# Kernel optimization log

Hardware: AMD Instinct MI355X
Metric: run time of the kernel (lower is better)

## Reference

```python
import jax, jax.numpy as jnp
import numpy as np

EPS = jnp.finfo(jnp.float32).eps


def setup_inputs() -> dict:
    key = jax.random.key(0)
    k0, k1, k2 = jax.random.split(key, 3)
    B, N = 1, 4194304
    cloud_t0 = jax.random.normal(k0, (B, N, 3), dtype=jnp.float32)
    cloud_t1 = jax.random.normal(k1, (B, N, 3), dtype=jnp.float32)
    weights = jax.random.uniform(k2, (B, N), dtype=jnp.float32)
    return {"cloud_t0": cloud_t0, "cloud_t1": cloud_t1, "weights": weights}


def reference(cloud_t0, cloud_t1, weights):
    # use_epsilon_on_weights = False branch
    count_nonzero = jnp.sum(weights > 0.0, axis=-1)
    not_enough_points = count_nonzero < 3
    weights = weights + (not_enough_points.astype(weights.dtype) * EPS)[:, None]

    cum_wts = jnp.sum(weights, axis=-1)                      # (B,)
    w = weights[:, :, None]                                   # (B,N,1)
    mx = jnp.sum(cloud_t0 * w, axis=1) / cum_wts[:, None]     # (B,3) weighted centroid
    my = jnp.sum(cloud_t1 * w, axis=1) / cum_wts[:, None]
    Xc = cloud_t0 - mx[:, None, :]
    Yc = cloud_t1 - my[:, None, :]
    # weighted cross-covariance: (B,3,3)
    Sxy = jnp.einsum('bno,bni->boi', Yc * w, Xc) / cum_wts[:, None, None]

    U, D, Vh = jnp.linalg.svd(Sxy, full_matrices=False)       # torch.svd returns V = Vh^T
    V = jnp.swapaxes(Vh, -1, -2)

    # rank via torch.linalg.matrix_rank default tol: max_sv * max(m,n) * eps
    tol = D.max(axis=-1) * 3 * EPS
    rank = jnp.sum(D > tol[:, None], axis=-1)

    det_S = jnp.linalg.det(Sxy)
    det_mul = jnp.linalg.det(U) * jnp.linalg.det(V)
    sign_full = jnp.where(det_S < 0.0, -1.0, 1.0)             # rank == 3 case
    sign_def = jnp.where(jnp.isclose(det_mul, -1.0), -1.0, 1.0)  # rank == 2 case
    s = jnp.where(rank > 2, sign_full, sign_def)              # (B,)

    # R = U @ diag(1,1,s) @ V^T
    diag = jnp.stack([jnp.ones_like(s), jnp.ones_like(s), s], axis=-1)  # (B,3)
    R = jnp.einsum('boc,bc,bic->boi', U, diag, V)             # (B,3,3)
    t = my - jnp.einsum('boc,bc->bo', R, mx)                  # (B,3)

    B = R.shape[0]
    R4 = jnp.concatenate([R, jnp.zeros((B, 1, 3), R.dtype)], axis=1)    # (B,4,3)
    t4 = jnp.concatenate([t, jnp.ones((B, 1), t.dtype)], axis=-1)       # (B,4)
    T = jnp.concatenate([R4, t4[:, :, None]], axis=-1)        # (B,4,4)
    return T, not_enough_points
```

## Files before the change

### kernel.cpp

```cpp
#include <hip/hip_runtime.h>
#include <math.h>

#define NACC 32

typedef float f4 __attribute__((ext_vector_type(4)));

__device__ __forceinline__ void accum_point(float w, float x0, float x1, float x2,
                                            float y0, float y1, float y2, float* a) {
    a[0] += (w > 0.0f) ? 1.0f : 0.0f;
    a[1] += w;
    a[2] = fmaf(w, x0, a[2]); a[3] = fmaf(w, x1, a[3]); a[4] = fmaf(w, x2, a[4]);
    float wy0 = w * y0, wy1 = w * y1, wy2 = w * y2;
    a[5] += wy0; a[6] += wy1; a[7] += wy2;
    a[8]  = fmaf(wy0, x0, a[8]);  a[9]  = fmaf(wy0, x1, a[9]);  a[10] = fmaf(wy0, x2, a[10]);
    a[11] = fmaf(wy1, x0, a[11]); a[12] = fmaf(wy1, x1, a[12]); a[13] = fmaf(wy1, x2, a[13]);
    a[14] = fmaf(wy2, x0, a[14]); a[15] = fmaf(wy2, x1, a[15]); a[16] = fmaf(wy2, x2, a[16]);
    a[17] += x0; a[18] += x1; a[19] += x2;
    a[20] += y0; a[21] += y1; a[22] += y2;
    a[23] = fmaf(y0, x0, a[23]); a[24] = fmaf(y0, x1, a[24]); a[25] = fmaf(y0, x2, a[25]);
    a[26] = fmaf(y1, x0, a[26]); a[27] = fmaf(y1, x1, a[27]); a[28] = fmaf(y1, x2, a[28]);
    a[29] = fmaf(y2, x0, a[29]); a[30] = fmaf(y2, x1, a[30]); a[31] = fmaf(y2, x2, a[31]);
}

__global__ __launch_bounds__(256) void kabsch_reduce(
    const float* __restrict__ c0, const float* __restrict__ c1,
    const float* __restrict__ w, int N, float* __restrict__ partials, int nblocks) {
    __shared__ float wred[4][NACC];

    float a[NACC];
    #pragma unroll
    for (int i = 0; i < NACC; ++i) a[i] = 0.0f;

    const int t = threadIdx.x;
    const int lane = t & 63, wave = t >> 6;
    const f4* __restrict__ A4 = (const f4*)c0;
    const f4* __restrict__ B4 = (const f4*)c1;
    const f4* __restrict__ W4 = (const f4*)w;

    const int ngrp = N >> 2;
    const int stride = gridDim.x << 8;
    for (int g = (blockIdx.x << 8) + t; g < ngrp; g += stride) {
        const f4* pa = A4 + 3 * (size_t)g;
        const f4* pb = B4 + 3 * (size_t)g;
        const f4* pw = W4 + (size_t)g;
        f4 a0, a1, a2, b0, b1, b2, vw;
        asm volatile("global_load_dwordx4 %0, %1, off"           : "=v"(a0) : "v"(pa));
        asm volatile("global_load_dwordx4 %0, %1, off offset:16" : "=v"(a1) : "v"(pa));
        asm volatile("global_load_dwordx4 %0, %1, off offset:32" : "=v"(a2) : "v"(pa));
        asm volatile("global_load_dwordx4 %0, %1, off"           : "=v"(b0) : "v"(pb));
        asm volatile("global_load_dwordx4 %0, %1, off offset:16" : "=v"(b1) : "v"(pb));
        asm volatile("global_load_dwordx4 %0, %1, off offset:32" : "=v"(b2) : "v"(pb));
        asm volatile("global_load_dwordx4 %0, %1, off"           : "=v"(vw) : "v"(pw));
        asm volatile("s_waitcnt vmcnt(0)" ::: "memory");
        __builtin_amdgcn_sched_barrier(0);
        accum_point(vw.x, a0.x, a0.y, a0.z, b0.x, b0.y, b0.z, a);
        accum_point(vw.y, a0.w, a1.x, a1.y, b0.w, b1.x, b1.y, a);
        accum_point(vw.z, a1.z, a1.w, a2.x, b1.z, b1.w, b2.x, a);
        accum_point(vw.w, a2.y, a2.z, a2.w, b2.y, b2.z, b2.w, a);
    }
    if (blockIdx.x == 0 && t == 0) {
        for (int i = (N >> 2) << 2; i < N; ++i)
            accum_point(w[i], c0[3*i], c0[3*i+1], c0[3*i+2],
                        c1[3*i], c1[3*i+1], c1[3*i+2], a);
    }

    {
        int hi;
        hi = lane & 1;
        #pragma unroll
        for (int i = 0; i < 16; ++i) {
            float send = hi ? a[i] : a[i + 16];
            float recv = __shfl_xor(send, 1, 64);
            a[i] = (hi ? a[i + 16] : a[i]) + recv;
        }
        hi = lane & 2;
        #pragma unroll
        for (int i = 0; i < 8; ++i) {
            float send = hi ? a[i] : a[i + 8];
            float recv = __shfl_xor(send, 2, 64);
            a[i] = (hi ? a[i + 8] : a[i]) + recv;
        }
        hi = lane & 4;
        #pragma unroll
        for (int i = 0; i < 4; ++i) {
            float send = hi ? a[i] : a[i + 4];
            float recv = __shfl_xor(send, 4, 64);
            a[i] = (hi ? a[i + 4] : a[i]) + recv;
        }
        hi = lane & 8;
        #pragma unroll
        for (int i = 0; i < 2; ++i) {
            float send = hi ? a[i] : a[i + 2];
            float recv = __shfl_xor(send, 8, 64);
            a[i] = (hi ? a[i + 2] : a[i]) + recv;
        }
        hi = lane & 16;
        {
            float send = hi ? a[0] : a[1];
            float recv = __shfl_xor(send, 16, 64);
            a[0] = (hi ? a[1] : a[0]) + recv;
        }
        a[0] += __shfl_xor(a[0], 32, 64);
    }
    if (lane < 32) {
        int acc = ((lane & 1) << 4) | ((lane & 2) << 2) | (lane & 4)
                | ((lane & 8) >> 2) | ((lane & 16) >> 4);
        wred[wave][acc] = a[0];
    }
    __syncthreads();
    if (t < NACC)
        partials[t * nblocks + blockIdx.x] =
            wred[0][t] + wred[1][t] + wred[2][t] + wred[3][t];
}

__device__ __forceinline__ double det3(const double m[3][3]) {
    return m[0][0] * (m[1][1] * m[2][2] - m[1][2] * m[2][1])
         - m[0][1] * (m[1][0] * m[2][2] - m[1][2] * m[2][0])
         + m[0][2] * (m[1][0] * m[2][1] - m[1][1] * m[2][0]);
}

__global__ __launch_bounds__(256) void kabsch_finalize(
    const float* __restrict__ partials, int nblocks, int N, float* __restrict__ out) {
    double d[NACC];
    #pragma unroll
    for (int i = 0; i < NACC; ++i) d[i] = 0.0;
    for (int m = threadIdx.x; m < nblocks; m += 256) {
        #pragma unroll
        for (int i = 0; i < NACC; ++i)
            d[i] += (double)partials[i * nblocks + m];
    }
    #pragma unroll
    for (int off = 32; off > 0; off >>= 1) {
        #pragma unroll
        for (int i = 0; i < NACC; ++i) d[i] += __shfl_down(d[i], off, 64);
    }
    __shared__ double sm[4][NACC];
    int wave = threadIdx.x >> 6, lane = threadIdx.x & 63;
    if (lane == 0) {
        #pragma unroll
        for (int i = 0; i < NACC; ++i) sm[wave][i] = d[i];
    }
    __syncthreads();
    if (threadIdx.x != 0) return;
    #pragma unroll
    for (int i = 0; i < NACC; ++i) d[i] = sm[0][i] + sm[1][i] + sm[2][i] + sm[3][i];

    const double EPSF = (double)1.1920929e-7f;
    double cnt = d[0];
    double W = d[1];
    double swx[3] = { d[2], d[3], d[4] };
    double swy[3] = { d[5], d[6], d[7] };
    double swyx[9];
    for (int i = 0; i < 9; ++i) swyx[i] = d[8 + i];
    bool nep = cnt < 3.0;
    if (nep) {
        W += EPSF * (double)N;
        for (int i = 0; i < 3; ++i) { swx[i] += EPSF * d[17 + i]; swy[i] += EPSF * d[20 + i]; }
        for (int i = 0; i < 9; ++i) swyx[i] += EPSF * d[23 + i];
    }

    double mx[3], my[3];
    for (int i = 0; i < 3; ++i) { mx[i] = swx[i] / W; my[i] = swy[i] / W; }
    double S[3][3];
    for (int o = 0; o < 3; ++o)
        for (int i = 0; i < 3; ++i)
            S[o][i] = swyx[o * 3 + i] / W - my[o] * mx[i];

    double Bm[3][3], V[3][3];
    for (int i = 0; i < 3; ++i)
        for (int j = 0; j < 3; ++j) {
            double acc = 0.0;
            for (int k = 0; k < 3; ++k) acc += S[k][i] * S[k][j];
            Bm[i][j] = acc;
            V[i][j] = (i == j) ? 1.0 : 0.0;
        }
    for (int sweep = 0; sweep < 30; ++sweep) {
        double off2 = Bm[0][1]*Bm[0][1] + Bm[0][2]*Bm[0][2] + Bm[1][2]*Bm[1][2];
        double diag2 = Bm[0][0]*Bm[0][0] + Bm[1][1]*Bm[1][1] + Bm[2][2]*Bm[2][2];
        if (off2 <= diag2 * 1e-32 + 1e-300) break;
        for (int pair = 0; pair < 3; ++pair) {
            int p = (pair == 2) ? 1 : 0;
            int q = (pair == 0) ? 1 : 2;
            double apq = Bm[p][q];
            if (fabs(apq) < 1e-300) continue;
            double theta = (Bm[q][q] - Bm[p][p]) / (2.0 * apq);
            double tt = ((theta >= 0.0) ? 1.0 : -1.0) / (fabs(theta) + sqrt(1.0 + theta * theta));
            double c = 1.0 / sqrt(1.0 + tt * tt);
            double sn = tt * c;
            for (int k = 0; k < 3; ++k) {
                double bkp = Bm[k][p], bkq = Bm[k][q];
                Bm[k][p] = c * bkp - sn * bkq;
                Bm[k][q] = sn * bkp + c * bkq;
            }
            for (int k = 0; k < 3; ++k) {
                double bpk = Bm[p][k], bqk = Bm[q][k];
                Bm[p][k] = c * bpk - sn * bqk;
                Bm[q][k] = sn * bpk + c * bqk;
            }
            for (int k = 0; k < 3; ++k) {
                double vkp = V[k][p], vkq = V[k][q];
                V[k][p] = c * vkp - sn * vkq;
                V[k][q] = sn * vkp + c * vkq;
            }
        }
    }
    double lam[3] = { Bm[0][0], Bm[1][1], Bm[2][2] };
    for (int i = 0; i < 2; ++i)
        for (int j = i + 1; j < 3; ++j)
            if (lam[j] > lam[i]) {
                double tl = lam[i]; lam[i] = lam[j]; lam[j] = tl;
                for (int k = 0; k < 3; ++k) { double tv = V[k][i]; V[k][i] = V[k][j]; V[k][j] = tv; }
            }
    double sig[3];
    for (int i = 0; i < 3; ++i) sig[i] = sqrt(fmax(lam[i], 0.0));

    double U[3][3];
    for (int i = 0; i < 3; ++i) {
        double u0 = S[0][0]*V[0][i] + S[0][1]*V[1][i] + S[0][2]*V[2][i];
        double u1 = S[1][0]*V[0][i] + S[1][1]*V[1][i] + S[1][2]*V[2][i];
        double u2 = S[2][0]*V[0][i] + S[2][1]*V[1][i] + S[2][2]*V[2][i];
        double nrm = sqrt(u0*u0 + u1*u1 + u2*u2);
        if (nrm > 1e-150) {
            U[0][i] = u0 / nrm; U[1][i] = u1 / nrm; U[2][i] = u2 / nrm;
        } else if (i == 0) {
            U[0][0] = 1.0; U[1][0] = 0.0; U[2][0] = 0.0;
        } else if (i == 1) {
            double e0 = (fabs(U[0][0]) < 0.9) ? 1.0 : 0.0;
            double e1 = 1.0 - e0;
            double dp = e0 * U[0][0] + e1 * U[1][0];
            double v0 = e0 - dp * U[0][0], v1 = e1 - dp * U[1][0], v2 = -dp * U[2][0];
            double n2 = sqrt(v0*v0 + v1*v1 + v2*v2);
            U[0][1] = v0 / n2; U[1][1] = v1 / n2; U[2][1] = v2 / n2;
        } else {
            U[0][2] = U[1][0]*U[2][1] - U[2][0]*U[1][1];
            U[1][2] = U[2][0]*U[0][1] - U[0][0]*U[2][1];
            U[2][2] = U[0][0]*U[1][1] - U[1][0]*U[0][1];
        }
    }

    double tol = sig[0] * 3.0 * EPSF;
    int rank = (sig[0] > tol) + (sig[1] > tol) + (sig[2] > tol);
    double detS = det3(S);
    double det_mul = det3(U) * det3(V);
    double sign_full = (detS < 0.0) ? -1.0 : 1.0;
    double sign_def = (fabs(det_mul + 1.0) <= 1.00001e-5) ? -1.0 : 1.0;
    double s = (rank > 2) ? sign_full : sign_def;

    double R[3][3];
    for (int o = 0; o < 3; ++o)
        for (int i = 0; i < 3; ++i)
            R[o][i] = U[o][0]*V[i][0] + U[o][1]*V[i][1] + s * U[o][2]*V[i][2];
    double tv[3];
    for (int o = 0; o < 3; ++o)
        tv[o] = my[o] - (R[o][0]*mx[0] + R[o][1]*mx[1] + R[o][2]*mx[2]);

    for (int o = 0; o < 3; ++o) {
        out[o * 4 + 0] = (float)R[o][0];
        out[o * 4 + 1] = (float)R[o][1];
        out[o * 4 + 2] = (float)R[o][2];
        out[o * 4 + 3] = (float)tv[o];
    }
    out[12] = 0.0f; out[13] = 0.0f; out[14] = 0.0f; out[15] = 1.0f;
    out[16] = nep ? 1.0f : 0.0f;
}

extern "C" void kernel_launch(void* const* d_in, const int* in_sizes, int n_in,
                              void* d_out, int out_size, void* d_ws, size_t ws_size,
                              hipStream_t stream) {
    const float* c0 = (const float*)d_in[0];
    const float* c1 = (const float*)d_in[1];
    const float* w  = (const float*)d_in[2];
    float* out = (float*)d_out;
    int N = in_sizes[2];

    int ngrp = N >> 2;
    int blocks = (ngrp + 255) >> 8;
    if (blocks > 4096) blocks = 4096;
    if (blocks < 1) blocks = 1;
    size_t need = (size_t)blocks * NACC * sizeof(float);
    if (need > ws_size) {
        blocks = (int)(ws_size / (NACC * sizeof(float)));
        if (blocks < 1) blocks = 1;
    }
    float* partials = (float*)d_ws;

    kabsch_reduce<<<blocks, 256, 0, stream>>>(c0, c1, w, N, partials, blocks);
    kabsch_finalize<<<1, 256, 0, stream>>>(partials, blocks, N, out);
}
```

Measured before the change: 155.3 us.

## Fuse reduce and finalize kernels with last-block ticket and parallel partial sum

```diff
diff --git a/kernel.cpp b/kernel.cpp
--- a/kernel.cpp
+++ b/kernel.cpp
@@ -22,9 +22,16 @@
     a[29] = fmaf(y2, x0, a[29]); a[30] = fmaf(y2, x1, a[30]); a[31] = fmaf(y2, x2, a[31]);
 }
 
-__global__ __launch_bounds__(256) void kabsch_reduce(
+__device__ __forceinline__ double det3(const double m[3][3]) {
+    return m[0][0] * (m[1][1] * m[2][2] - m[1][2] * m[2][1])
+         - m[0][1] * (m[1][0] * m[2][2] - m[1][2] * m[2][0])
+         + m[0][2] * (m[1][0] * m[2][1] - m[1][1] * m[2][0]);
+}
+
+__global__ __launch_bounds__(256) void kabsch_fused(
     const float* __restrict__ c0, const float* __restrict__ c1,
-    const float* __restrict__ w, int N, float* __restrict__ partials, int nblocks) {
+    const float* __restrict__ w, int N, float* __restrict__ partials, int nblocks,
+    unsigned* __restrict__ ticket, float* __restrict__ out) {
     __shared__ float wred[4][NACC];
 
     float a[NACC];
@@ -111,39 +118,53 @@
     if (t < NACC)
         partials[t * nblocks + blockIdx.x] =
             wred[0][t] + wred[1][t] + wred[2][t] + wred[3][t];
-}
-
-__device__ __forceinline__ double det3(const double m[3][3]) {
-    return m[0][0] * (m[1][1] * m[2][2] - m[1][2] * m[2][1])
-         - m[0][1] * (m[1][0] * m[2][2] - m[1][2] * m[2][0])
-         + m[0][2] * (m[1][0] * m[2][1] - m[1][1] * m[2][0]);
-}
-
-__global__ __launch_bounds__(256) void kabsch_finalize(
-    const float* __restrict__ partials, int nblocks, int N, float* __restrict__ out) {
+
+    __threadfence();
+    __syncthreads();
+    __shared__ unsigned amlast;
+    if (t == 0) amlast = atomicAdd(ticket, 1u);
+    __syncthreads();
+    if (amlast != (unsigned)(nblocks - 1)) return;
+    __threadfence();
+
+    double dd[8];
+    #pragma unroll
+    for (int i = 0; i < 8; ++i) dd[i] = 0.0;
+    if ((nblocks & 3) == 0) {
+        const int nb4 = nblocks >> 2;
+        const f4* __restrict__ p4 = (const f4*)partials;
+        #pragma unroll
+        for (int i = 0; i < 8; ++i) {
+            int row = (wave << 3) + i;
+            for (int j = lane; j < nb4; j += 64) {
+                f4 v = p4[row * nb4 + j];
+                dd[i] += ((double)v.x + (double)v.y) + ((double)v.z + (double)v.w);
+            }
+        }
+    } else {
+        #pragma unroll
+        for (int i = 0; i < 8; ++i) {
+            int row = (wave << 3) + i;
+            for (int j = lane; j < nblocks; j += 64)
+                dd[i] += (double)partials[row * nblocks + j];
+        }
+    }
+    #pragma unroll
+    for (int off = 32; off > 0; off >>= 1) {
+        #pragma unroll
+        for (int i = 0; i < 8; ++i) dd[i] += __shfl_down(dd[i], off, 64);
+    }
+    __shared__ double sm[NACC];
+    if (lane == 0) {
+        #pragma unroll
+        for (int i = 0; i < 8; ++i) sm[(wave << 3) + i] = dd[i];
+    }
+    __syncthreads();
+    if (t != 0) return;
+
     double d[NACC];
     #pragma unroll
-    for (int i = 0; i < NACC; ++i) d[i] = 0.0;
-    for (int m = threadIdx.x; m < nblocks; m += 256) {
-        #pragma unroll
-        for (int i = 0; i < NACC; ++i)
-            d[i] += (double)partials[i * nblocks + m];
-    }
-    #pragma unroll
-    for (int off = 32; off > 0; off >>= 1) {
-        #pragma unroll
-        for (int i = 0; i < NACC; ++i) d[i] += __shfl_down(d[i], off, 64);
-    }
-    __shared__ double sm[4][NACC];
-    int wave = threadIdx.x >> 6, lane = threadIdx.x & 63;
-    if (lane == 0) {
-        #pragma unroll
-        for (int i = 0; i < NACC; ++i) sm[wave][i] = d[i];
-    }
-    __syncthreads();
-    if (threadIdx.x != 0) return;
-    #pragma unroll
-    for (int i = 0; i < NACC; ++i) d[i] = sm[0][i] + sm[1][i] + sm[2][i] + sm[3][i];
+    for (int i = 0; i < NACC; ++i) d[i] = sm[i];
 
     const double EPSF = (double)1.1920929e-7f;
     double cnt = d[0];
@@ -275,15 +296,16 @@
 
     int ngrp = N >> 2;
     int blocks = (ngrp + 255) >> 8;
-    if (blocks > 4096) blocks = 4096;
+    if (blocks > 1024) blocks = 1024;
     if (blocks < 1) blocks = 1;
-    size_t need = (size_t)blocks * NACC * sizeof(float);
+    size_t need = (size_t)blocks * NACC * sizeof(float) + sizeof(unsigned);
     if (need > ws_size) {
-        blocks = (int)(ws_size / (NACC * sizeof(float)));
+        blocks = (int)((ws_size - sizeof(unsigned)) / (NACC * sizeof(float)));
         if (blocks < 1) blocks = 1;
     }
     float* partials = (float*)d_ws;
-
-    kabsch_reduce<<<blocks, 256, 0, stream>>>(c0, c1, w, N, partials, blocks);
-    kabsch_finalize<<<1, 256, 0, stream>>>(partials, blocks, N, out);
+    unsigned* ticket = (unsigned*)((char*)d_ws + (size_t)blocks * NACC * sizeof(float));
+
+    hipMemsetAsync(ticket, 0, sizeof(unsigned), stream);
+    kabsch_fused<<<blocks, 256, 0, stream>>>(c0, c1, w, N, partials, blocks, ticket, out);
 }
```

After: 308.7 us. +98.8%, slower.
